# Performance work log

Measured on AMD Instinct MI355X. Metric: run time of the kernel, lower is better.

The kernel has to match this reference:

```python
import jax, jax.numpy as jnp
import numpy as np

D_MODEL = 2048
N_HEADS = 16
HEAD_DIM = 128
WINDOW = 256
B, T = 2, 2048
SCALE = float(np.sqrt(HEAD_DIM))


def setup_inputs() -> dict:
    key = jax.random.key(0)
    ks = jax.random.split(key, 5)
    init = 0.02
    x = jax.random.normal(ks[0], (B, T, D_MODEL), dtype=jnp.float32)
    Wq = jax.random.normal(ks[1], (D_MODEL, D_MODEL), dtype=jnp.float32) * init
    Wk = jax.random.normal(ks[2], (D_MODEL, D_MODEL), dtype=jnp.float32) * init
    Wv = jax.random.normal(ks[3], (D_MODEL, D_MODEL), dtype=jnp.float32) * init
    Wo = jax.random.normal(ks[4], (D_MODEL, D_MODEL), dtype=jnp.float32) * init
    return {"x": x, "Wq": Wq, "Wk": Wk, "Wv": Wv, "Wo": Wo}


def _allowed_mask():
    # [H, T, T] bool: global (even) heads -> causal; local (odd) heads -> causal band of WINDOW
    idx = jnp.arange(T)
    causal = idx[None, :] <= idx[:, None]                      # [T, T]
    band = idx[None, :] >= (idx[:, None] - WINDOW + 1)         # [T, T]
    is_global = (jnp.arange(N_HEADS) % 2) == 0                 # [H]
    return causal[None] & (is_global[:, None, None] | band[None])


def reference(x, Wq, Wk, Wv, Wo):
    # projections (nn.Linear: y = x @ W.T), reshape to [B, H, T, D]
    def proj(W):
        return (x @ W.T).reshape(B, T, N_HEADS, HEAD_DIM).transpose(0, 2, 1, 3)

    q, k, v = proj(Wq), proj(Wk), proj(Wv)
    scores = jnp.einsum("bhtd,bhsd->bhts", q, k) / SCALE       # [B, H, T, T]
    allowed = _allowed_mask()                                  # [H, T, T]
    neg_inf = jnp.asarray(-jnp.inf, dtype=scores.dtype)
    scores = jnp.where(allowed[None], scores, neg_inf)
    attn = jax.nn.softmax(scores, axis=-1)
    out = jnp.einsum("bhts,bhsd->bhtd", attn, v)               # [B, H, T, D]
    concat = out.transpose(0, 2, 1, 3).reshape(B, T, N_HEADS * HEAD_DIM)
    return concat @ Wo.T
```

## Files before the change

### kernel.cpp

```cpp
#include <hip/hip_runtime.h>

typedef __attribute__((ext_vector_type(4))) float f32x4;
typedef __attribute__((ext_vector_type(8))) short bf16x8;
typedef __attribute__((ext_vector_type(4))) unsigned short u16x4;
typedef unsigned short u16;

#define MFMA16(a, b, c) __builtin_amdgcn_mfma_f32_16x16x32_bf16((a), (b), (c), 0, 0, 0)

#define T_SEQ 2048
#define DMODEL 2048
#define NHEADS 16
#define HDIM 128
#define WINDOW 256
#define MROWS 4096
#define SC 0.08838834764831845f

__device__ __forceinline__ u16 f2bf(float f) {
  union { float f; unsigned u; } v; v.f = f;
  return (u16)((v.u + 0x7FFFu + ((v.u >> 16) & 1u)) >> 16);
}
__device__ __forceinline__ float bf2f(u16 u) {
  union { unsigned u; float f; } v; v.u = ((unsigned)u) << 16;
  return v.f;
}
__device__ __forceinline__ void gl_lds16(const u16* g, u16* l) {
  __builtin_amdgcn_global_load_lds((const __attribute__((address_space(1))) void*)(g),
                                   (__attribute__((address_space(3))) void*)(l), 16, 0, 0);
}

#define BAR __builtin_amdgcn_s_barrier()
#define FEN asm volatile("" ::: "memory")
#define VMC3 asm volatile("s_waitcnt vmcnt(3)" ::: "memory")
#define VMC2 asm volatile("s_waitcnt vmcnt(2)" ::: "memory")
#define VMC0 asm volatile("s_waitcnt vmcnt(0)" ::: "memory")

__global__ __launch_bounds__(256) void convert_all(const float* __restrict__ x,
                                                   const float* __restrict__ wq,
                                                   const float* __restrict__ wk,
                                                   const float* __restrict__ wv,
                                                   const float* __restrict__ wo,
                                                   u16* __restrict__ dst) {
  const size_t NX = (size_t)MROWS * DMODEL;
  const size_t NW = (size_t)DMODEL * DMODEL;
  const size_t chunks = (NX + 4 * NW) / 8;
  for (size_t ci = (size_t)blockIdx.x * 256 + threadIdx.x; ci < chunks;
       ci += (size_t)gridDim.x * 256) {
    const size_t off = ci * 8;
    const float* src;
    size_t so;
    if (off < NX) { src = x; so = off; }
    else {
      size_t rem = off - NX;
      if (rem < NW) { src = wq; so = rem; }
      else if (rem < 2 * NW) { src = wk; so = rem - NW; }
      else if (rem < 3 * NW) { src = wv; so = rem - 2 * NW; }
      else { src = wo; so = rem - 3 * NW; }
    }
    f32x4 a = *(const f32x4*)&src[so];
    f32x4 b = *(const f32x4*)&src[so + 4];
    bf16x8 o;
#pragma unroll
    for (int j = 0; j < 4; ++j) { o[j] = (short)f2bf(a[j]); o[j + 4] = (short)f2bf(b[j]); }
    *(bf16x8*)&dst[off] = o;
  }
}

__global__ __launch_bounds__(512, 2) void gemm_qkv(const u16* __restrict__ A,
                                                   const u16* __restrict__ W,
                                                   u16* __restrict__ qk,
                                                   u16* __restrict__ vt) {
  __shared__ u16 lds[57344];
  const int tid = threadIdx.x, w = tid >> 6, lane = tid & 63;
  const int wm = w >> 2, wn = w & 3;
  const int fr = lane & 15, g = lane >> 4, g4 = g * 4;

  const int xcd = blockIdx.x & 7, bi = blockIdx.x >> 3;
  const int mt = bi >> 2, nt = xcd * 4 + (bi & 3);
  const int m0 = mt * 256, n0 = nt * 192;

  const int xs0 = (g ^ (fr & 7)) * 8;
  const int xs1 = xs0 ^ 32;
  const int aRow = wm * 128 + fr;
  const int bRow = wn * 48 + fr;

  const int sr = tid >> 3;
  const int scc = ((tid & 7) ^ (sr & 7)) * 8;
  const u16* pA0  = A + (size_t)(m0 + sr) * DMODEL + scc;
  const u16* pA1  = A + (size_t)(m0 + 64 + sr) * DMODEL + scc;
  const u16* pB0  = W + (size_t)(n0 + sr) * DMODEL + scc;
  const u16* pB0b = W + (size_t)(n0 + 64 + sr) * DMODEL + scc;
  const u16* pB1  = W + (size_t)(n0 + 128 + sr) * DMODEL + scc;

#define SAH(h, t, c)                                                                   \
  { gl_lds16(pA0 + (size_t)(h) * 128 * DMODEL + (t) * 64,                              \
             &lds[(c) * 16384 + (h) * 8192 + w * 512]);                                \
    gl_lds16(pA1 + (size_t)(h) * 128 * DMODEL + (t) * 64,                              \
             &lds[(c) * 16384 + (h) * 8192 + 4096 + w * 512]); }
#define SBH0(t, c)                                                                     \
  { gl_lds16(pB0 + (size_t)(t) * 64, &lds[32768 + (c) * 12288 + w * 512]);             \
    gl_lds16(pB0b + (size_t)(t) * 64, &lds[32768 + (c) * 12288 + 4096 + w * 512]); }
#define SBH1(t, c)                                                                     \
  { gl_lds16(pB1 + (size_t)(t) * 64, &lds[32768 + (c) * 12288 + 8192 + w * 512]); }

#define RD_AL(c)                                                                       \
  { _Pragma("unroll") for (int m_ = 0; m_ < 4; ++m_) {                                 \
      af[m_][0] = *(const bf16x8*)&lds[(c) * 16384 + (aRow + m_ * 16) * 64 + xs0];     \
      af[m_][1] = *(const bf16x8*)&lds[(c) * 16384 + (aRow + m_ * 16) * 64 + xs1]; } }
#define RD_AH(c)                                                                       \
  { _Pragma("unroll") for (int m_ = 0; m_ < 4; ++m_) {                                 \
      af[m_][0] = *(const bf16x8*)&lds[(c) * 16384 + (aRow + 64 + m_ * 16) * 64 + xs0];\
      af[m_][1] = *(const bf16x8*)&lds[(c) * 16384 + (aRow + 64 + m_ * 16) * 64 + xs1]; } }
#define RD_B(c)                                                                        \
  { _Pragma("unroll") for (int n_ = 0; n_ < 3; ++n_) {                                 \
      bfr[n_][0] = *(const bf16x8*)&lds[32768 + (c) * 12288 + (bRow + n_ * 16) * 64 + xs0]; \
      bfr[n_][1] = *(const bf16x8*)&lds[32768 + (c) * 12288 + (bRow + n_ * 16) * 64 + xs1]; } }

#define MMQ(MB)                                                                        \
  { __builtin_amdgcn_s_setprio(1);                                                    \
    _Pragma("unroll") for (int kc_ = 0; kc_ < 2; ++kc_)                                \
      _Pragma("unroll") for (int m_ = 0; m_ < 4; ++m_)                                 \
        _Pragma("unroll") for (int n_ = 0; n_ < 3; ++n_)                               \
          acc[(MB) + m_][n_] = MFMA16(af[m_][kc_], bfr[n_][kc_], acc[(MB) + m_][n_]);  \
    __builtin_amdgcn_s_setprio(0); }

  bf16x8 af[4][2], bfr[3][2];
  f32x4 acc[8][3];
#pragma unroll
  for (int i = 0; i < 8; ++i)
#pragma unroll
    for (int j = 0; j < 3; ++j) acc[i][j] = (f32x4){0.f, 0.f, 0.f, 0.f};

  SAH(0, 0, 0); SAH(1, 0, 0);
  SBH0(0, 0); SBH1(0, 0);
  SBH0(1, 1); SBH1(1, 1);
  VMC3; BAR;

#pragma unroll 1
  for (int i = 0; i < 15; ++i) {
    const int t0 = 2 * i;
    RD_AL(0); RD_B(0); SAH(0, t0 + 1, 1); SAH(1, t0 + 1, 1);
    FEN; BAR; MMQ(0); FEN; BAR;
    RD_AH(0); SBH0(t0 + 2, 0); SBH1(t0 + 2, 0);
    VMC3; BAR; MMQ(4); FEN; BAR;
    RD_AL(1); RD_B(1); SAH(0, t0 + 2, 0); SAH(1, t0 + 2, 0);
    FEN; BAR; MMQ(0); FEN; BAR;
    RD_AH(1); SBH0(t0 + 3, 1); SBH1(t0 + 3, 1);
    VMC3; BAR; MMQ(4); FEN; BAR;
  }
  RD_AL(0); RD_B(0); SAH(0, 31, 1); SAH(1, 31, 1);
  FEN; BAR; MMQ(0); FEN; BAR;
  RD_AH(0);
  VMC0; BAR; MMQ(4); FEN; BAR;
  RD_AL(1); RD_B(1);
  FEN; BAR; MMQ(0); FEN; BAR;
  RD_AH(1);
  FEN; BAR; MMQ(4);

#pragma unroll
  for (int mi = 0; mi < 8; ++mi)
#pragma unroll
    for (int ni = 0; ni < 3; ++ni) {
      const int row0 = m0 + wm * 128 + mi * 16 + g4;
      const int cg = n0 + wn * 48 + ni * 16 + fr;
      if (cg < 2 * DMODEL) {
#pragma unroll
        for (int r = 0; r < 4; ++r)
          qk[(size_t)(row0 + r) * (2 * DMODEL) + cg] = f2bf(acc[mi][ni][r]);
      } else {
        const int cc = cg - 2 * DMODEL;
        const int hh = cc >> 7, d = cc & 127;
        const int bb = row0 >> 11, tl = row0 & 2047;
        u16x4 w4;
#pragma unroll
        for (int r = 0; r < 4; ++r) w4[r] = f2bf(acc[mi][ni][r]);
        *(u16x4*)&vt[((size_t)(bb * NHEADS + hh) * HDIM + d) * T_SEQ + tl] = w4;
      }
    }
#undef SAH
#undef SBH0
#undef SBH1
#undef RD_AL
#undef RD_AH
#undef RD_B
#undef MMQ
}

__global__ __launch_bounds__(512, 2) void gemm_out(const u16* __restrict__ A,
                                                   const u16* __restrict__ W0,
                                                   float* __restrict__ outf) {
  __shared__ u16 lds2[49152];
  const int tid = threadIdx.x, w = tid >> 6, lane = tid & 63;
  const int wm = w >> 2, wn = w & 3;
  const int fr = lane & 15, g = lane >> 4, g4 = g * 4;

  const int xcd = blockIdx.x & 7, bi = blockIdx.x >> 3;
  const int mt = bi >> 1, nt = xcd * 2 + (bi & 1);
  const int m0 = mt * 256, n0 = nt * 128;

  const int xs0 = (g ^ (fr & 7)) * 8;
  const int xs1 = xs0 ^ 32;
  const int aRow = wm * 128 + fr;
  const int bRow = wn * 32 + fr;

  const int sr = tid >> 3;
  const int scc = ((tid & 7) ^ (sr & 7)) * 8;
  const u16* pA0  = A + (size_t)(m0 + sr) * DMODEL + scc;
  const u16* pA1  = A + (size_t)(m0 + 64 + sr) * DMODEL + scc;
  const u16* pB0  = W0 + (size_t)(n0 + sr) * DMODEL + scc;
  const u16* pB0b = W0 + (size_t)(n0 + 64 + sr) * DMODEL + scc;

#define S2A(h, t, c)                                                                   \
  { gl_lds16(pA0 + (size_t)(h) * 128 * DMODEL + (t) * 64,                              \
             &lds2[(c) * 16384 + (h) * 8192 + w * 512]);                               \
    gl_lds16(pA1 + (size_t)(h) * 128 * DMODEL + (t) * 64,                              \
             &lds2[(c) * 16384 + (h) * 8192 + 4096 + w * 512]); }
#define S2B(t, c)                                                                      \
  { gl_lds16(pB0 + (size_t)(t) * 64, &lds2[32768 + (c) * 8192 + w * 512]);             \
    gl_lds16(pB0b + (size_t)(t) * 64, &lds2[32768 + (c) * 8192 + 4096 + w * 512]); }

#define R2AL(c)                                                                        \
  { _Pragma("unroll") for (int m_ = 0; m_ < 4; ++m_) {                                 \
      af[m_][0] = *(const bf16x8*)&lds2[(c) * 16384 + (aRow + m_ * 16) * 64 + xs0];    \
      af[m_][1] = *(const bf16x8*)&lds2[(c) * 16384 + (aRow + m_ * 16) * 64 + xs1]; } }
#define R2AH(c)                                                                        \
  { _Pragma("unroll") for (int m_ = 0; m_ < 4; ++m_) {                                 \
      af[m_][0] = *(const bf16x8*)&lds2[(c) * 16384 + (aRow + 64 + m_ * 16) * 64 + xs0]; \
      af[m_][1] = *(const bf16x8*)&lds2[(c) * 16384 + (aRow + 64 + m_ * 16) * 64 + xs1]; } }
#define R2B(c)                                                                         \
  { _Pragma("unroll") for (int n_ = 0; n_ < 2; ++n_) {                                 \
      bfr[n_][0] = *(const bf16x8*)&lds2[32768 + (c) * 8192 + (bRow + n_ * 16) * 64 + xs0]; \
      bfr[n_][1] = *(const bf16x8*)&lds2[32768 + (c) * 8192 + (bRow + n_ * 16) * 64 + xs1]; } }

#define M2(MB)                                                                         \
  { __builtin_amdgcn_s_setprio(1);                                                    \
    _Pragma("unroll") for (int kc_ = 0; kc_ < 2; ++kc_)                                \
      _Pragma("unroll") for (int m_ = 0; m_ < 4; ++m_)                                 \
        _Pragma("unroll") for (int n_ = 0; n_ < 2; ++n_)                               \
          acc[(MB) + m_][n_] = MFMA16(af[m_][kc_], bfr[n_][kc_], acc[(MB) + m_][n_]);  \
    __builtin_amdgcn_s_setprio(0); }

  bf16x8 af[4][2], bfr[2][2];
  f32x4 acc[8][2];
#pragma unroll
  for (int i = 0; i < 8; ++i)
#pragma unroll
    for (int j = 0; j < 2; ++j) acc[i][j] = (f32x4){0.f, 0.f, 0.f, 0.f};

  S2A(0, 0, 0); S2A(1, 0, 0);
  S2B(0, 0);
  S2B(1, 1);
  VMC2; BAR;

#pragma unroll 1
  for (int i = 0; i < 15; ++i) {
    const int t0 = 2 * i;
    R2AL(0); R2B(0); S2A(0, t0 + 1, 1); S2A(1, t0 + 1, 1);
    FEN; BAR; M2(0); FEN; BAR;
    R2AH(0); S2B(t0 + 2, 0);
    VMC2; BAR; M2(4); FEN; BAR;
    R2AL(1); R2B(1); S2A(0, t0 + 2, 0); S2A(1, t0 + 2, 0);
    FEN; BAR; M2(0); FEN; BAR;
    R2AH(1); S2B(t0 + 3, 1);
    VMC2; BAR; M2(4); FEN; BAR;
  }
  R2AL(0); R2B(0); S2A(0, 31, 1); S2A(1, 31, 1);
  FEN; BAR; M2(0); FEN; BAR;
  R2AH(0);
  VMC0; BAR; M2(4); FEN; BAR;
  R2AL(1); R2B(1);
  FEN; BAR; M2(0); FEN; BAR;
  R2AH(1);
  FEN; BAR; M2(4);

#pragma unroll
  for (int mi = 0; mi < 8; ++mi)
#pragma unroll
    for (int ni = 0; ni < 2; ++ni) {
      const int row0 = m0 + wm * 128 + mi * 16 + g4;
      const int c = n0 + wn * 32 + ni * 16 + fr;
#pragma unroll
      for (int r = 0; r < 4; ++r)
        outf[(size_t)(row0 + r) * DMODEL + c] = acc[mi][ni][r];
    }
#undef S2A
#undef S2B
#undef R2AL
#undef R2AH
#undef R2B
#undef M2
}

#define QB 128
#define KVB 64
#define LDK 136
#define LDV 72
#define LDP 80

__global__ __launch_bounds__(512) void attn_kernel(const u16* __restrict__ qk,
                                                   const u16* __restrict__ vt,
                                                   u16* __restrict__ op,
                                                   u16* __restrict__ pO,
                                                   float* __restrict__ pm,
                                                   float* __restrict__ pl) {
  __shared__ u16 Ks[KVB][LDK];
  __shared__ u16 Vs[HDIM][LDV];
  __shared__ u16 Ps[8][16][LDP];

  const int bx = blockIdx.x, h = blockIdx.y, b = blockIdx.z;
  const bool isglobal = (h & 1) == 0;
  int qt, klo, khi, part = 0;
  bool partial = false;
  if (isglobal) {
    if (bx < 16) {
      qt = 15 - (bx >> 1);
      part = bx & 1;
      partial = true;
      if (part == 0) { klo = 0; khi = 15; } else { klo = 16; khi = 2 * qt + 1; }
    } else {
      qt = 23 - bx;
      klo = 0; khi = 2 * qt + 1;
    }
  } else {
    if (bx >= 16) return;
    qt = 15 - bx;
    const int lo_ = qt * QB - (WINDOW - 1);
    klo = lo_ > 0 ? (lo_ >> 6) : 0;
    khi = 2 * qt + 1;
  }

  const int tid = threadIdx.x, wave = tid >> 6, lane = tid & 63;
  const int fr = lane & 15, ko = (lane >> 4) * 8, g4 = (lane >> 4) * 4;
  const int q0 = qt * QB;
  const size_t baseq = (size_t)b * T_SEQ * (2 * DMODEL) + (size_t)h * HDIM;
  const size_t basek = baseq + DMODEL;
  const size_t basev = (size_t)(b * NHEADS + h) * HDIM * T_SEQ;
  const size_t baseo = (size_t)b * T_SEQ * DMODEL + (size_t)h * HDIM;

  bf16x8 qf[4];
  {
    const int qrow = q0 + wave * 16 + fr;
#pragma unroll
    for (int ds = 0; ds < 4; ++ds)
      qf[ds] = *(const bf16x8*)&qk[baseq + (size_t)qrow * (2 * DMODEL) + ds * 32 + ko];
  }

  float mrun = -1e30f, lrun = 0.f;
  f32x4 o[8];
#pragma unroll
  for (int dt = 0; dt < 8; ++dt) o[dt] = (f32x4){0.f, 0.f, 0.f, 0.f};

  const int kr = tid >> 4, kc = (tid & 15) * 8;
  const int vr = tid >> 3, vc = (tid & 7) * 8;
  bf16x8 kreg[2], vreg[2];

#define LOADTILE(KT)                                                                      \
  {                                                                                       \
    _Pragma("unroll") for (int it = 0; it < 2; ++it) {                                    \
      kreg[it] = *(const bf16x8*)&qk[basek + (size_t)((KT) * KVB + kr + it * 32) * (2 * DMODEL) + kc]; \
      vreg[it] = *(const bf16x8*)&vt[basev + (size_t)(vr + it * 64) * T_SEQ + (KT) * KVB + vc];        \
    }                                                                                     \
  }
#define WRITETILE()                                                                       \
  {                                                                                       \
    _Pragma("unroll") for (int it = 0; it < 2; ++it) {                                    \
      *(bf16x8*)&Ks[kr + it * 32][kc] = kreg[it];                                         \
      *(bf16x8*)&Vs[vr + it * 64][vc] = vreg[it];                                         \
    }                                                                                     \
  }

  LOADTILE(klo);
  WRITETILE();
  __syncthreads();

  const int qg = q0 + wave * 16 + fr;

  for (int kt = klo; kt <= khi; ++kt) {
    const bool more = kt < khi;
    if (more) LOADTILE(kt + 1);

    f32x4 s[4];
    __builtin_amdgcn_s_setprio(1);
#pragma unroll
    for (int kk = 0; kk < 4; ++kk) {
      f32x4 a = (f32x4){0.f, 0.f, 0.f, 0.f};
#pragma unroll
      for (int ds = 0; ds < 4; ++ds) {
        bf16x8 kf = *(const bf16x8*)&Ks[kk * 16 + fr][ds * 32 + ko];
        a = MFMA16(kf, qf[ds], a);
      }
      s[kk] = a;
    }
    __builtin_amdgcn_s_setprio(0);

    float sv[16];
    float pmax = -1e30f;
#pragma unroll
    for (int kk = 0; kk < 4; ++kk)
#pragma unroll
      for (int reg = 0; reg < 4; ++reg) {
        const int cg = kt * KVB + kk * 16 + g4 + reg;
        const bool allowed = (cg <= qg) && (isglobal || cg >= qg - (WINDOW - 1));
        const float v = allowed ? s[kk][reg] : -1e30f;
        sv[kk * 4 + reg] = v;
        pmax = fmaxf(pmax, v);
      }
    pmax = fmaxf(pmax, __shfl_xor(pmax, 16, 64));
    pmax = fmaxf(pmax, __shfl_xor(pmax, 32, 64));
    const float nm = fmaxf(mrun, pmax);
    const float fac = __expf((mrun - nm) * SC);
    mrun = nm;
    float rs = 0.f;
    u16 pb[16];
#pragma unroll
    for (int i = 0; i < 16; ++i) {
      const float p = (sv[i] > -5e29f) ? __expf((sv[i] - nm) * SC) : 0.f;
      rs += p;
      pb[i] = f2bf(p);
    }
    rs += __shfl_xor(rs, 16, 64);
    rs += __shfl_xor(rs, 32, 64);
    lrun = lrun * fac + rs;

#pragma unroll
    for (int kk = 0; kk < 4; ++kk) {
      u16x4 wv;
      wv[0] = pb[kk * 4]; wv[1] = pb[kk * 4 + 1]; wv[2] = pb[kk * 4 + 2]; wv[3] = pb[kk * 4 + 3];
      *(u16x4*)&Ps[wave][fr][kk * 16 + g4] = wv;
    }

    float ff[4];
#pragma unroll
    for (int r = 0; r < 4; ++r) ff[r] = __shfl(fac, g4 + r, 64);
#pragma unroll
    for (int dt = 0; dt < 8; ++dt)
#pragma unroll
      for (int r = 0; r < 4; ++r) o[dt][r] *= ff[r];

    bf16x8 pf0 = *(const bf16x8*)&Ps[wave][fr][ko];
    bf16x8 pf1 = *(const bf16x8*)&Ps[wave][fr][32 + ko];
    __builtin_amdgcn_s_setprio(1);
#pragma unroll
    for (int dt = 0; dt < 8; ++dt) {
      bf16x8 vf0 = *(const bf16x8*)&Vs[dt * 16 + fr][ko];
      bf16x8 vf1 = *(const bf16x8*)&Vs[dt * 16 + fr][32 + ko];
      o[dt] = MFMA16(pf0, vf0, o[dt]);
      o[dt] = MFMA16(pf1, vf1, o[dt]);
    }
    __builtin_amdgcn_s_setprio(0);

    __syncthreads();
    if (more) WRITETILE();
    __syncthreads();
  }

  if (!partial) {
    const float inv = 1.0f / lrun;
    float iv[4];
#pragma unroll
    for (int r = 0; r < 4; ++r) iv[r] = __shfl(inv, g4 + r, 64);
#pragma unroll
    for (int r = 0; r < 4; ++r) {
      const int qrow = q0 + wave * 16 + g4 + r;
#pragma unroll
      for (int dt = 0; dt < 8; ++dt)
        op[baseo + (size_t)qrow * DMODEL + dt * 16 + fr] = f2bf(o[dt][r] * iv[r]);
    }
  } else {
    const int sidx = (((b * 8 + (h >> 1)) * 8 + (qt - 8)) << 1) + part;
    const size_t sb = (size_t)sidx * QB;
#pragma unroll
    for (int r = 0; r < 4; ++r) {
      const size_t row = sb + wave * 16 + g4 + r;
#pragma unroll
      for (int dt = 0; dt < 8; ++dt)
        pO[row * HDIM + dt * 16 + fr] = f2bf(o[dt][r]);
    }
    if (lane < 16) {
      pm[sb + wave * 16 + lane] = mrun;
      pl[sb + wave * 16 + lane] = lrun;
    }
  }
}

__global__ __launch_bounds__(256) void merge_kernel(const u16* __restrict__ pO,
                                                    const float* __restrict__ pm,
                                                    const float* __restrict__ pl,
                                                    u16* __restrict__ op) {
  const int x = blockIdx.x;
  if (x >= 128) return;
  const int qt8 = x & 7, eh = (x >> 3) & 7, b = x >> 6;
  const int h = eh * 2, qt = 8 + qt8;
  const int s0 = x * 2, s1 = s0 + 1;

  for (int i = 0; i < 8; ++i) {
    const int vidx = threadIdx.x + i * 256;
    const int row = vidx >> 4, d8 = (vidx & 15) * 8;
    const float m0 = pm[s0 * QB + row], m1 = pm[s1 * QB + row];
    const float l0 = pl[s0 * QB + row], l1 = pl[s1 * QB + row];
    const float m = fmaxf(m0, m1);
    const float w0 = __expf((m0 - m) * SC), w1 = __expf((m1 - m) * SC);
    const float inv = 1.0f / (l0 * w0 + l1 * w1);
    bf16x8 a = *(const bf16x8*)&pO[((size_t)s0 * QB + row) * HDIM + d8];
    bf16x8 c = *(const bf16x8*)&pO[((size_t)s1 * QB + row) * HDIM + d8];
    bf16x8 r;
#pragma unroll
    for (int j = 0; j < 8; ++j)
      r[j] = (short)f2bf((bf2f((u16)a[j]) * w0 + bf2f((u16)c[j]) * w1) * inv);
    *(bf16x8*)&op[((size_t)(b * T_SEQ + qt * QB + row)) * DMODEL + h * HDIM + d8] = r;
  }
}

extern "C" void kernel_launch(void* const* d_in, const int* in_sizes, int n_in,
                              void* d_out, int out_size, void* d_ws, size_t ws_size,
                              hipStream_t stream) {
  (void)in_sizes; (void)n_in; (void)out_size; (void)ws_size;
  const float* x  = (const float*)d_in[0];
  const float* Wq = (const float*)d_in[1];
  const float* Wk = (const float*)d_in[2];
  const float* Wv = (const float*)d_in[3];
  const float* Wo = (const float*)d_in[4];

  const size_t NX = (size_t)MROWS * DMODEL;
  const size_t NW = (size_t)DMODEL * DMODEL;
  u16* ws  = (u16*)d_ws;
  u16* xb  = ws;
  u16* wqb = ws + NX;
  u16* wkb = wqb + NW;
  u16* wvb = wkb + NW;
  u16* wob = wvb + NW;
  u16* qkb = wob + NW;
  u16* vtb = qkb + (size_t)MROWS * 2 * DMODEL;

  u16*   pO = wqb;
  float* pm = (float*)(wqb + (size_t)256 * QB * HDIM);
  float* pl = pm + 256 * QB;

  convert_all<<<2048, 256, 0, stream>>>(x, Wq, Wk, Wv, Wo, ws);

  gemm_qkv<<<512, 512, 0, stream>>>(xb, wqb, qkb, vtb);

  attn_kernel<<<dim3(24, NHEADS, 2), 512, 0, stream>>>(qkb, vtb, xb, pO, pm, pl);

  merge_kernel<<<128, 256, 0, stream>>>(pO, pm, pl, xb);

  gemm_out<<<256, 512, 0, stream>>>(xb, wob, (float*)d_out);
}
```

Before: 258.8 us.

## Double-buffer attention K/V tiles via direct global-to-LDS loads with XOR swizzle

Rewrites the attention kernel's K/V staging so tiles are loaded directly from global memory into a double-buffered LDS region, using XOR-swizzled layouts instead of padded arrays. This drops the register round trip and one of the two per-iteration barriers. It also adds a lazy online-softmax rescale that skips the max update and the O rescale when the block max grows by less than a threshold. The launch bounds now request 4 waves per SIMD, and the merge kernel's bounds guard is removed. This relies on the gl_lds16, VMC0, FEN and BAR helpers being defined elsewhere, and the lazy rescale could risk overflow if the threshold is wrong.

```diff
diff --git a/kernel.cpp b/kernel.cpp
--- a/kernel.cpp
+++ b/kernel.cpp
@@ -292,19 +292,14 @@
 
 #define QB 128
 #define KVB 64
-#define LDK 136
-#define LDV 72
-#define LDP 80
-
-__global__ __launch_bounds__(512) void attn_kernel(const u16* __restrict__ qk,
-                                                   const u16* __restrict__ vt,
-                                                   u16* __restrict__ op,
-                                                   u16* __restrict__ pO,
-                                                   float* __restrict__ pm,
-                                                   float* __restrict__ pl) {
-  __shared__ u16 Ks[KVB][LDK];
-  __shared__ u16 Vs[HDIM][LDV];
-  __shared__ u16 Ps[8][16][LDP];
+
+__global__ __launch_bounds__(512, 4) void attn_kernel(const u16* __restrict__ qk,
+                                                      const u16* __restrict__ vt,
+                                                      u16* __restrict__ op,
+                                                      u16* __restrict__ pO,
+                                                      float* __restrict__ pm,
+                                                      float* __restrict__ pl) {
+  __shared__ u16 lds[40960];
 
   const int bx = blockIdx.x, h = blockIdx.y, b = blockIdx.z;
   const bool isglobal = (h & 1) == 0;
@@ -329,7 +324,8 @@
   }
 
   const int tid = threadIdx.x, wave = tid >> 6, lane = tid & 63;
-  const int fr = lane & 15, ko = (lane >> 4) * 8, g4 = (lane >> 4) * 4;
+  const int fr = lane & 15, g = lane >> 4, g4 = g * 4;
+  const int xk = fr & 7;
   const int q0 = qt * QB;
   const size_t baseq = (size_t)b * T_SEQ * (2 * DMODEL) + (size_t)h * HDIM;
   const size_t basek = baseq + DMODEL;
@@ -341,7 +337,7 @@
     const int qrow = q0 + wave * 16 + fr;
 #pragma unroll
     for (int ds = 0; ds < 4; ++ds)
-      qf[ds] = *(const bf16x8*)&qk[baseq + (size_t)qrow * (2 * DMODEL) + ds * 32 + ko];
+      qf[ds] = *(const bf16x8*)&qk[baseq + (size_t)qrow * (2 * DMODEL) + ds * 32 + g * 8];
   }
 
   float mrun = -1e30f, lrun = 0.f;
@@ -349,34 +345,35 @@
 #pragma unroll
   for (int dt = 0; dt < 8; ++dt) o[dt] = (f32x4){0.f, 0.f, 0.f, 0.f};
 
-  const int kr = tid >> 4, kc = (tid & 15) * 8;
-  const int vr = tid >> 3, vc = (tid & 7) * 8;
-  bf16x8 kreg[2], vreg[2];
-
-#define LOADTILE(KT)                                                                      \
-  {                                                                                       \
-    _Pragma("unroll") for (int it = 0; it < 2; ++it) {                                    \
-      kreg[it] = *(const bf16x8*)&qk[basek + (size_t)((KT) * KVB + kr + it * 32) * (2 * DMODEL) + kc]; \
-      vreg[it] = *(const bf16x8*)&vt[basev + (size_t)(vr + it * 64) * T_SEQ + (KT) * KVB + vc];        \
-    }                                                                                     \
-  }
-#define WRITETILE()                                                                       \
-  {                                                                                       \
-    _Pragma("unroll") for (int it = 0; it < 2; ++it) {                                    \
-      *(bf16x8*)&Ks[kr + it * 32][kc] = kreg[it];                                         \
-      *(bf16x8*)&Vs[vr + it * 64][vc] = vreg[it];                                         \
-    }                                                                                     \
-  }
-
-  LOADTILE(klo);
-  WRITETILE();
-  __syncthreads();
-
+  const int j0 = wave * 2, j1 = wave * 2 + 1;
+  const int gi0 = j0 * 64 + lane, gi1 = j1 * 64 + lane;
+  const int kr0 = gi0 >> 4, kc0 = (gi0 & 15) ^ (kr0 & 7);
+  const int kr1 = gi1 >> 4, kc1 = (gi1 & 15) ^ (kr1 & 7);
+  const u16* pK0 = qk + basek + (size_t)kr0 * (2 * DMODEL) + kc0 * 8;
+  const u16* pK1 = qk + basek + (size_t)kr1 * (2 * DMODEL) + kc1 * 8;
+  const int d0 = gi0 >> 3, vs0 = (gi0 & 7) ^ (d0 & 7);
+  const int d1 = gi1 >> 3, vs1 = (gi1 & 7) ^ (d1 & 7);
+  const u16* pV0 = vt + basev + (size_t)d0 * T_SEQ + vs0 * 8;
+  const u16* pV1 = vt + basev + (size_t)d1 * T_SEQ + vs1 * 8;
+
+#define STAGE(KT, c)                                                                   \
+  { gl_lds16(pK0 + (size_t)(KT) * (KVB * 2 * DMODEL), &lds[(c) * 8192 + j0 * 512]);    \
+    gl_lds16(pK1 + (size_t)(KT) * (KVB * 2 * DMODEL), &lds[(c) * 8192 + j1 * 512]);    \
+    gl_lds16(pV0 + (KT) * KVB, &lds[16384 + (c) * 8192 + j0 * 512]);                   \
+    gl_lds16(pV1 + (KT) * KVB, &lds[16384 + (c) * 8192 + j1 * 512]); }
+
+  u16* Pw = &lds[32768 + wave * 1024];
   const int qg = q0 + wave * 16 + fr;
 
+  STAGE(klo, klo & 1);
+  VMC0; BAR;
+
   for (int kt = klo; kt <= khi; ++kt) {
+    const int c = kt & 1;
     const bool more = kt < khi;
-    if (more) LOADTILE(kt + 1);
+    if (more) STAGE(kt + 1, c ^ 1);
+    const u16* Kc = &lds[c * 8192];
+    const u16* Vc = &lds[16384 + c * 8192];
 
     f32x4 s[4];
     __builtin_amdgcn_s_setprio(1);
@@ -385,7 +382,8 @@
       f32x4 a = (f32x4){0.f, 0.f, 0.f, 0.f};
 #pragma unroll
       for (int ds = 0; ds < 4; ++ds) {
-        bf16x8 kf = *(const bf16x8*)&Ks[kk * 16 + fr][ds * 32 + ko];
+        const int r = kk * 16 + fr;
+        bf16x8 kf = *(const bf16x8*)&Kc[r * 128 + (((ds * 4 + g) ^ xk) << 3)];
         a = MFMA16(kf, qf[ds], a);
       }
       s[kk] = a;
@@ -406,14 +404,18 @@
       }
     pmax = fmaxf(pmax, __shfl_xor(pmax, 16, 64));
     pmax = fmaxf(pmax, __shfl_xor(pmax, 32, 64));
-    const float nm = fmaxf(mrun, pmax);
-    const float fac = __expf((mrun - nm) * SC);
-    mrun = nm;
+    const bool resc = !__all(pmax - mrun <= 90.5f);
+    float fac = 1.f;
+    if (resc) {
+      const float nm = fmaxf(mrun, pmax);
+      fac = __expf((mrun - nm) * SC);
+      mrun = nm;
+    }
     float rs = 0.f;
     u16 pb[16];
 #pragma unroll
     for (int i = 0; i < 16; ++i) {
-      const float p = (sv[i] > -5e29f) ? __expf((sv[i] - nm) * SC) : 0.f;
+      const float p = (sv[i] > -5e29f) ? __expf((sv[i] - mrun) * SC) : 0.f;
       rs += p;
       pb[i] = f2bf(p);
     }
@@ -425,32 +427,35 @@
     for (int kk = 0; kk < 4; ++kk) {
       u16x4 wv;
       wv[0] = pb[kk * 4]; wv[1] = pb[kk * 4 + 1]; wv[2] = pb[kk * 4 + 2]; wv[3] = pb[kk * 4 + 3];
-      *(u16x4*)&Ps[wave][fr][kk * 16 + g4] = wv;
-    }
-
-    float ff[4];
-#pragma unroll
-    for (int r = 0; r < 4; ++r) ff[r] = __shfl(fac, g4 + r, 64);
-#pragma unroll
-    for (int dt = 0; dt < 8; ++dt)
-#pragma unroll
-      for (int r = 0; r < 4; ++r) o[dt][r] *= ff[r];
-
-    bf16x8 pf0 = *(const bf16x8*)&Ps[wave][fr][ko];
-    bf16x8 pf1 = *(const bf16x8*)&Ps[wave][fr][32 + ko];
+      *(u16x4*)&Pw[fr * 64 + (((2 * kk + (g >> 1)) ^ xk) << 3) + (g & 1) * 4] = wv;
+    }
+
+    if (resc) {
+      float ff[4];
+#pragma unroll
+      for (int r = 0; r < 4; ++r) ff[r] = __shfl(fac, g4 + r, 64);
+#pragma unroll
+      for (int dt = 0; dt < 8; ++dt)
+#pragma unroll
+        for (int r = 0; r < 4; ++r) o[dt][r] *= ff[r];
+    }
+
+    bf16x8 pf0 = *(const bf16x8*)&Pw[fr * 64 + ((g ^ xk) << 3)];
+    bf16x8 pf1 = *(const bf16x8*)&Pw[fr * 64 + (((4 + g) ^ xk) << 3)];
     __builtin_amdgcn_s_setprio(1);
 #pragma unroll
     for (int dt = 0; dt < 8; ++dt) {
-      bf16x8 vf0 = *(const bf16x8*)&Vs[dt * 16 + fr][ko];
-      bf16x8 vf1 = *(const bf16x8*)&Vs[dt * 16 + fr][32 + ko];
+      const int d = dt * 16 + fr;
+      bf16x8 vf0 = *(const bf16x8*)&Vc[d * 64 + ((g ^ xk) << 3)];
+      bf16x8 vf1 = *(const bf16x8*)&Vc[d * 64 + (((4 + g) ^ xk) << 3)];
       o[dt] = MFMA16(pf0, vf0, o[dt]);
       o[dt] = MFMA16(pf1, vf1, o[dt]);
     }
     __builtin_amdgcn_s_setprio(0);
 
-    __syncthreads();
-    if (more) WRITETILE();
-    __syncthreads();
+    FEN;
+    VMC0;
+    BAR;
   }
 
   if (!partial) {
@@ -480,6 +485,7 @@
       pl[sb + wave * 16 + lane] = lrun;
     }
   }
+#undef STAGE
 }
 
 __global__ __launch_bounds__(256) void merge_kernel(const u16* __restrict__ pO,
@@ -487,7 +493,6 @@
                                                     const float* __restrict__ pl,
                                                     u16* __restrict__ op) {
   const int x = blockIdx.x;
-  if (x >= 128) return;
   const int qt8 = x & 7, eh = (x >> 3) & 7, b = x >> 6;
   const int h = eh * 2, qt = 8 + qt8;
   const int s0 = x * 2, s1 = s0 + 1;
```

Measured after the change: 250.1 us. 3.4% less time.
